# Kernel tuning notes

Hardware: AMD Instinct MI355X
Metric: run time of the kernel (lower is better)

The kernel has to match this reference:

```python
import jax, jax.numpy as jnp
import numpy as np
import math


def setup_inputs() -> dict:
    key = jax.random.key(0)
    ks = jax.random.split(key, 16)
    B, S, H, K, PREV = 32, 2048, 1024, 4, 2
    sc = 0.02
    return {
        "last_hidden": jax.random.normal(ks[0], (1, B, H), jnp.float32),
        "decoder_inputs": jax.random.normal(ks[1], (B, 1, H), jnp.float32),
        "encoder_outputs": jax.random.normal(ks[2], (B, S, H), jnp.float32),
        "attention_scores": jax.random.normal(ks[3], (PREV, B, 1, S), jnp.float32),
        "attention_mask": jnp.zeros((B, 1, S), jnp.float32),
        "evidence_scores": jax.random.uniform(ks[4], (B,), jnp.float32),
        "evidence_sentence_index": jax.random.randint(ks[5], (B, PREV), 0, S, dtype=jnp.int32),
        "W_ih": jax.random.normal(ks[6], (3 * H, H), jnp.float32) * sc,
        "W_hh": jax.random.normal(ks[7], (3 * H, H), jnp.float32) * sc,
        "b_ih": jax.random.normal(ks[8], (3 * H,), jnp.float32) * sc,
        "b_hh": jax.random.normal(ks[9], (3 * H,), jnp.float32) * sc,
        "Wk": jax.random.normal(ks[10], (H, H), jnp.float32) * sc,
        "bk": jnp.zeros((H,), jnp.float32),
        "Wv": jax.random.normal(ks[11], (H, H), jnp.float32) * sc,
        "bv": jnp.zeros((H,), jnp.float32),
        "topk": K,
    }


def _gru_step(x, h, W_ih, W_hh, b_ih, b_hh):
    # x, h: (B, H). PyTorch GRU cell math.
    gi = x @ W_ih.T + b_ih  # (B, 3H)
    gh = h @ W_hh.T + b_hh  # (B, 3H)
    i_r, i_z, i_n = jnp.split(gi, 3, axis=1)
    h_r, h_z, h_n = jnp.split(gh, 3, axis=1)
    r = jax.nn.sigmoid(i_r + h_r)
    z = jax.nn.sigmoid(i_z + h_z)
    n = jnp.tanh(i_n + r * h_n)
    return (1.0 - z) * n + z * h


def reference(last_hidden, decoder_inputs, encoder_outputs, attention_scores,
              attention_mask, evidence_scores, evidence_sentence_index,
              W_ih, W_hh, b_ih, b_hh, Wk, bk, Wv, bv, topk):
    B, S, H = encoder_outputs.shape
    K = topk
    R = B // K  # real batch (beam groups)

    key_eo = encoder_outputs @ Wk.T + bk    # (B, S, H)
    val_eo = encoder_outputs @ Wv.T + bv    # (B, S, H)

    h_new = _gru_step(decoder_inputs[:, 0], last_hidden[0], W_ih, W_hh, b_ih, b_hh)  # (B, H)
    output = h_new[:, None, :]              # (B, 1, H)

    attn_outputs = jnp.einsum('bih,bsh->bis', output, key_eo) / math.sqrt(H) + attention_mask  # (B,1,S)
    attn_alignment = jax.nn.softmax(attn_outputs, axis=-1)
    context = jnp.einsum('bis,bsh->bih', attn_alignment, val_eo)  # (B, 1, H)

    # top-k per beam, then joint rerank over topk*topk candidates per real example
    vals, idx = jax.lax.top_k(attn_alignment.reshape(R, K, S), K)  # (R, K, K), sorted desc
    scores = vals.reshape(B, K)
    sentences = idx.reshape(B, K)
    log_scores = -jnp.log(scores) + evidence_scores[:, None]       # (B, K)

    flat = log_scores.reshape(R, K * K)
    order = jnp.argsort(flat, axis=-1)[:, :K]                      # (R, K) ascending, stable
    new_evidence_scores = jnp.take_along_axis(flat, order, axis=1).reshape(B)
    s_flat = (order // K + jnp.arange(R)[:, None] * K).reshape(B)  # source beam in [0, B)
    r_flat = (order % K).reshape(B)

    sel_sent = sentences[s_flat, r_flat]                           # (B,)
    result = context[s_flat]                                       # (B, 1, H)
    hidden = h_new[s_flat][None]                                   # (1, B, H)
    new_evidence_sentence_index = jnp.concatenate(
        [evidence_sentence_index[s_flat], sel_sent[:, None].astype(evidence_sentence_index.dtype)], axis=1)
    new_attention_scores = jnp.concatenate(
        [attention_scores[:, s_flat], attn_outputs[s_flat][None]], axis=0)  # (prev+1, B, 1, S)
    new_attention_mask = attention_mask[s_flat]                    # (B, 1, S)

    return (result, hidden, new_evidence_sentence_index,
            new_attention_scores, new_attention_mask, new_evidence_scores)
```

## Files before the change

kernel.cpp:

```cpp
#include <hip/hip_runtime.h>
#include <hip/hip_bf16.h>
#include <cfloat>
#include <climits>
#include <cmath>

#define BB 32
#define SS 2048
#define HH 1024
#define KK 4
#define CH 32

__global__ __launch_bounds__(256) void gates_partial(
    const float* __restrict__ x, const float* __restrict__ h_old,
    const float* __restrict__ W_ih, const float* __restrict__ W_hh,
    float* __restrict__ part) {
  int t = threadIdx.x;
  int jb = blockIdx.x;
  int k0 = blockIdx.y * 64;
  bool second = (jb >= 12);
  const float* A = second ? h_old : x;
  const float* W = second ? W_hh : W_ih;
  int j0 = jb * 256;
  int jr = j0 - (second ? 3072 : 0);
  const float* wp = W + (size_t)(jr + t) * HH + k0;
  float acc[32];
#pragma unroll
  for (int b = 0; b < 32; b++) acc[b] = 0.f;
  for (int kk = 0; kk < 64; kk += 4) {
    float4 wv = *(const float4*)(wp + kk);
#pragma unroll
    for (int b = 0; b < 32; b++) {
      float4 a = *(const float4*)(A + (size_t)b * HH + k0 + kk);
      acc[b] += a.x * wv.x + a.y * wv.y + a.z * wv.z + a.w * wv.w;
    }
  }
  float* pb = part + (size_t)blockIdx.y * (32 * 6144) + j0 + t;
#pragma unroll
  for (int b = 0; b < 32; b++) pb[(size_t)b * 6144] = acc[b];
}

__global__ __launch_bounds__(256) void gru_q(
    const float* __restrict__ part, const float* __restrict__ b_ih,
    const float* __restrict__ b_hh, const float* __restrict__ h_old,
    const float* __restrict__ Wk, float* __restrict__ h_new,
    float* __restrict__ qpart2) {
  __shared__ float hs[256];
  int t = threadIdx.x;
  int kc = blockIdx.x, b = blockIdx.y;
  int h = kc * 256 + t;
  float s0 = 0.f, s1 = 0.f, s2 = 0.f, s3 = 0.f, s4 = 0.f, s5 = 0.f;
#pragma unroll
  for (int c = 0; c < 16; c++) {
    const float* p = part + ((size_t)c * 32 + b) * 6144;
    s0 += p[h];
    s1 += p[1024 + h];
    s2 += p[2048 + h];
    s3 += p[3072 + h];
    s4 += p[4096 + h];
    s5 += p[5120 + h];
  }
  float ir = s0 + b_ih[h], iz = s1 + b_ih[1024 + h], in_ = s2 + b_ih[2048 + h];
  float hr = s3 + b_hh[h], hz = s4 + b_hh[1024 + h], hn = s5 + b_hh[2048 + h];
  float r = 1.f / (1.f + expf(-(ir + hr)));
  float z = 1.f / (1.f + expf(-(iz + hz)));
  float n = tanhf(in_ + r * hn);
  float hv = (1.f - z) * n + z * h_old[b * HH + h];
  h_new[b * HH + h] = hv;
  hs[t] = hv;
  __syncthreads();
  float4 acc = make_float4(0.f, 0.f, 0.f, 0.f);
  const float* wbase = Wk + (size_t)kc * 256 * HH + 4 * t;
  for (int k = 0; k < 256; k += 4) {
    float4 w0 = *(const float4*)(wbase + (size_t)(k + 0) * HH);
    float4 w1 = *(const float4*)(wbase + (size_t)(k + 1) * HH);
    float4 w2 = *(const float4*)(wbase + (size_t)(k + 2) * HH);
    float4 w3 = *(const float4*)(wbase + (size_t)(k + 3) * HH);
    float a0 = hs[k], a1 = hs[k + 1], a2 = hs[k + 2], a3 = hs[k + 3];
    acc.x += a0 * w0.x + a1 * w1.x + a2 * w2.x + a3 * w3.x;
    acc.y += a0 * w0.y + a1 * w1.y + a2 * w2.y + a3 * w3.y;
    acc.z += a0 * w0.z + a1 * w1.z + a2 * w2.z + a3 * w3.z;
    acc.w += a0 * w0.w + a1 * w1.w + a2 * w2.w + a3 * w3.w;
  }
  *(float4*)(qpart2 + ((size_t)b * 4 + kc) * HH + 4 * t) = acc;
}

__global__ __launch_bounds__(256, 4) void fused_attn(
    const float* __restrict__ eo, const float* __restrict__ qpart2,
    const float* __restrict__ h_new, const float* __restrict__ bk,
    const float* __restrict__ mask, float* __restrict__ logits,
    float* __restrict__ c0part, float* __restrict__ msum_part) {
  __shared__ float q_lds[HH];
  __shared__ float wred[4];
  __shared__ float cacc[4][1024];
  __shared__ float cms[4][2];
  int b = blockIdx.y, sc = blockIdx.x, t = threadIdx.x;
  int w = t >> 6, lane = t & 63;
  {
    float4 qs = *(const float4*)(qpart2 + ((size_t)b * 4 + 0) * HH + 4 * t);
#pragma unroll
    for (int kc = 1; kc < 4; kc++) {
      float4 v = *(const float4*)(qpart2 + ((size_t)b * 4 + kc) * HH + 4 * t);
      qs.x += v.x; qs.y += v.y; qs.z += v.z; qs.w += v.w;
    }
    *(float4*)&q_lds[4 * t] = qs;
    float4 hv = *(const float4*)(h_new + (size_t)b * HH + 4 * t);
    float4 kv = *(const float4*)(bk + 4 * t);
    float p = hv.x * kv.x + hv.y * kv.y + hv.z * kv.z + hv.w * kv.w;
#pragma unroll
    for (int off = 32; off; off >>= 1) p += __shfl_xor(p, off);
    if (lane == 0) wred[w] = p;
  }
  __syncthreads();
  float hb = wred[0] + wred[1] + wred[2] + wred[3];
  float4 qv[4];
#pragma unroll
  for (int i = 0; i < 4; i++) qv[i] = *(const float4*)&q_lds[(i * 64 + lane) * 4];

  float m = -FLT_MAX, sum = 0.f;
  float4 acc[4];
#pragma unroll
  for (int i = 0; i < 4; i++) acc[i] = make_float4(0.f, 0.f, 0.f, 0.f);
  int rbase = sc * 64 + w * 16;
  for (int tile = 0; tile < 8; tile++) {
    int r0 = rbase + tile * 2;
    float4 rv[2][4];
#pragma unroll
    for (int rr = 0; rr < 2; rr++) {
      const float4* e4 = (const float4*)(eo + ((size_t)b * SS + r0 + rr) * HH);
#pragma unroll
      for (int i = 0; i < 4; i++) rv[rr][i] = e4[i * 64 + lane];
    }
    float p0 = 0.f, p1 = 0.f;
#pragma unroll
    for (int i = 0; i < 4; i++) {
      p0 += rv[0][i].x * qv[i].x + rv[0][i].y * qv[i].y +
            rv[0][i].z * qv[i].z + rv[0][i].w * qv[i].w;
      p1 += rv[1][i].x * qv[i].x + rv[1][i].y * qv[i].y +
            rv[1][i].z * qv[i].z + rv[1][i].w * qv[i].w;
    }
#pragma unroll
    for (int off = 32; off; off >>= 1) {
      p0 += __shfl_xor(p0, off);
      p1 += __shfl_xor(p1, off);
    }
    float lv0 = (p0 + hb) * 0.03125f + mask[(size_t)b * SS + r0];
    float lv1 = (p1 + hb) * 0.03125f + mask[(size_t)b * SS + r0 + 1];
    if (lane == 0) {
      logits[(size_t)b * SS + r0] = lv0;
      logits[(size_t)b * SS + r0 + 1] = lv1;
    }
    float m_new = fmaxf(m, fmaxf(lv0, lv1));
    float scale = expf(m - m_new);
    float w0 = expf(lv0 - m_new), w1 = expf(lv1 - m_new);
    sum = sum * scale + w0 + w1;
#pragma unroll
    for (int i = 0; i < 4; i++) {
      acc[i].x = acc[i].x * scale + w0 * rv[0][i].x + w1 * rv[1][i].x;
      acc[i].y = acc[i].y * scale + w0 * rv[0][i].y + w1 * rv[1][i].y;
      acc[i].z = acc[i].z * scale + w0 * rv[0][i].z + w1 * rv[1][i].z;
      acc[i].w = acc[i].w * scale + w0 * rv[0][i].w + w1 * rv[1][i].w;
    }
    m = m_new;
  }
#pragma unroll
  for (int i = 0; i < 4; i++) *(float4*)&cacc[w][i * 256 + lane * 4] = acc[i];
  if (lane == 0) { cms[w][0] = m; cms[w][1] = sum; }
  __syncthreads();
  float m0 = cms[0][0], m1 = cms[1][0], m2 = cms[2][0], m3 = cms[3][0];
  float mb = fmaxf(fmaxf(m0, m1), fmaxf(m2, m3));
  float wt0 = expf(m0 - mb), wt1 = expf(m1 - mb), wt2 = expf(m2 - mb),
        wt3 = expf(m3 - mb);
  float sb = cms[0][1] * wt0 + cms[1][1] * wt1 + cms[2][1] * wt2 + cms[3][1] * wt3;
  float4 a0 = *(float4*)&cacc[0][4 * t];
  float4 a1 = *(float4*)&cacc[1][4 * t];
  float4 a2 = *(float4*)&cacc[2][4 * t];
  float4 a3 = *(float4*)&cacc[3][4 * t];
  float4 r;
  r.x = wt0 * a0.x + wt1 * a1.x + wt2 * a2.x + wt3 * a3.x;
  r.y = wt0 * a0.y + wt1 * a1.y + wt2 * a2.y + wt3 * a3.y;
  r.z = wt0 * a0.z + wt1 * a1.z + wt2 * a2.z + wt3 * a3.z;
  r.w = wt0 * a0.w + wt1 * a1.w + wt2 * a2.w + wt3 * a3.w;
  *(float4*)(c0part + ((size_t)sc * 32 + b) * 1024 + 4 * t) = r;
  if (t == 0) {
    msum_part[((size_t)sc * 32 + b) * 2 + 0] = mb;
    msum_part[((size_t)sc * 32 + b) * 2 + 1] = sb;
  }
}

__device__ __forceinline__ bool vi_better(float av, int ai, float bv, int bi) {
  return av > bv || (av == bv && ai < bi);
}

__global__ __launch_bounds__(256) void attn_finish(
    const float* __restrict__ c0part, const float* __restrict__ msum_part,
    const float* __restrict__ logits, float* __restrict__ c0,
    float* __restrict__ scores, int* __restrict__ sent) {
  int b = blockIdx.x, t = threadIdx.x;
  float m = -FLT_MAX;
  float ms[CH];
#pragma unroll
  for (int c = 0; c < CH; c++) {
    ms[c] = msum_part[((size_t)c * 32 + b) * 2 + 0];
    m = fmaxf(m, ms[c]);
  }
  float sum = 0.f;
  float wc[CH];
#pragma unroll
  for (int c = 0; c < CH; c++) {
    wc[c] = expf(ms[c] - m);
    sum += msum_part[((size_t)c * 32 + b) * 2 + 1] * wc[c];
  }
  float inv = 1.f / sum;
  float4 a = make_float4(0.f, 0.f, 0.f, 0.f);
#pragma unroll
  for (int c = 0; c < CH; c++) {
    float4 v = *(const float4*)(c0part + ((size_t)c * 32 + b) * 1024 + 4 * t);
    a.x += wc[c] * v.x; a.y += wc[c] * v.y;
    a.z += wc[c] * v.z; a.w += wc[c] * v.w;
  }
  a.x *= inv; a.y *= inv; a.z *= inv; a.w *= inv;
  *(float4*)(c0 + (size_t)b * HH + 4 * t) = a;

  float tv0 = -FLT_MAX, tv1 = -FLT_MAX, tv2 = -FLT_MAX, tv3 = -FLT_MAX;
  int ti0 = INT_MAX, ti1 = INT_MAX, ti2 = INT_MAX, ti3 = INT_MAX;
#pragma unroll
  for (int it = 0; it < 8; it++) {
    int idx = it * 256 + t;
    float v = logits[(size_t)b * SS + idx];
    if (vi_better(v, idx, tv3, ti3)) {
      tv3 = v; ti3 = idx;
      if (vi_better(tv3, ti3, tv2, ti2)) { float fv = tv2; int fi = ti2; tv2 = tv3; ti2 = ti3; tv3 = fv; ti3 = fi; }
      if (vi_better(tv2, ti2, tv1, ti1)) { float fv = tv1; int fi = ti1; tv1 = tv2; ti1 = ti2; tv2 = fv; ti2 = fi; }
      if (vi_better(tv1, ti1, tv0, ti0)) { float fv = tv0; int fi = ti0; tv0 = tv1; ti0 = ti1; tv1 = fv; ti1 = fi; }
    }
  }
  __shared__ float sv[256][4];
  __shared__ int si[256][4];
  sv[t][0] = tv0; sv[t][1] = tv1; sv[t][2] = tv2; sv[t][3] = tv3;
  si[t][0] = ti0; si[t][1] = ti1; si[t][2] = ti2; si[t][3] = ti3;
  __syncthreads();
  for (int off = 128; off; off >>= 1) {
    if (t < off) {
      float bv0 = sv[t + off][0], bv1 = sv[t + off][1], bv2 = sv[t + off][2], bv3 = sv[t + off][3];
      int bi0 = si[t + off][0], bi1 = si[t + off][1], bi2 = si[t + off][2], bi3 = si[t + off][3];
      float mv0, mv1, mv2, mv3; int mi0, mi1, mi2, mi3;
      if (vi_better(tv0, ti0, bv3, bi3)) { mv0 = tv0; mi0 = ti0; } else { mv0 = bv3; mi0 = bi3; }
      if (vi_better(tv1, ti1, bv2, bi2)) { mv1 = tv1; mi1 = ti1; } else { mv1 = bv2; mi1 = bi2; }
      if (vi_better(tv2, ti2, bv1, bi1)) { mv2 = tv2; mi2 = ti2; } else { mv2 = bv1; mi2 = bi1; }
      if (vi_better(tv3, ti3, bv0, bi0)) { mv3 = tv3; mi3 = ti3; } else { mv3 = bv0; mi3 = bi0; }
      if (!vi_better(mv0, mi0, mv2, mi2)) { float fv = mv0; int fi = mi0; mv0 = mv2; mi0 = mi2; mv2 = fv; mi2 = fi; }
      if (!vi_better(mv1, mi1, mv3, mi3)) { float fv = mv1; int fi = mi1; mv1 = mv3; mi1 = mi3; mv3 = fv; mi3 = fi; }
      if (!vi_better(mv0, mi0, mv1, mi1)) { float fv = mv0; int fi = mi0; mv0 = mv1; mi0 = mi1; mv1 = fv; mi1 = fi; }
      if (!vi_better(mv2, mi2, mv3, mi3)) { float fv = mv2; int fi = mi2; mv2 = mv3; mi2 = mi3; mv3 = fv; mi3 = fi; }
      tv0 = mv0; tv1 = mv1; tv2 = mv2; tv3 = mv3;
      ti0 = mi0; ti1 = mi1; ti2 = mi2; ti3 = mi3;
      sv[t][0] = tv0; sv[t][1] = tv1; sv[t][2] = tv2; sv[t][3] = tv3;
      si[t][0] = ti0; si[t][1] = ti1; si[t][2] = ti2; si[t][3] = ti3;
    }
    __syncthreads();
  }
  if (t == 0) {
    scores[b * KK + 0] = expf(tv0 - m) * inv; sent[b * KK + 0] = ti0;
    scores[b * KK + 1] = expf(tv1 - m) * inv; sent[b * KK + 1] = ti1;
    scores[b * KK + 2] = expf(tv2 - m) * inv; sent[b * KK + 2] = ti2;
    scores[b * KK + 3] = expf(tv3 - m) * inv; sent[b * KK + 3] = ti3;
  }
}

__global__ __launch_bounds__(256) void ctx_sel_gather(
    const float* __restrict__ scores, const int* __restrict__ sent,
    const float* __restrict__ evidence, const int* __restrict__ esi,
    const float* __restrict__ Wv, const float* __restrict__ bvec,
    const float* __restrict__ c0, const float* __restrict__ hnew,
    const float* __restrict__ attn_in, const float* __restrict__ logits,
    const float* __restrict__ mask, float* __restrict__ out0,
    float* __restrict__ out1, float* __restrict__ out2,
    float* __restrict__ out3, float* __restrict__ out4,
    float* __restrict__ out5) {
  __shared__ int s_sh;
  int jq = blockIdx.x, b = blockIdx.y, t = threadIdx.x;
  int w = t >> 6, lane = t & 63;
  if (t == 0) {
    int r = b >> 2, j = b & 3;
    float ls[16];
    bool used[16];
    for (int k1 = 0; k1 < 4; k1++)
      for (int k2 = 0; k2 < 4; k2++)
        ls[k1 * 4 + k2] = -logf(scores[(r * 4 + k1) * 4 + k2]) + evidence[r * 4 + k1];
    for (int i = 0; i < 16; i++) used[i] = false;
    int best = 0;
    float bvv = FLT_MAX;
    for (int jj = 0; jj <= j; jj++) {
      best = 0;
      bvv = FLT_MAX;
      for (int i = 0; i < 16; i++)
        if (!used[i] && ls[i] < bvv) { bvv = ls[i]; best = i; }
      used[best] = true;
    }
    int k1 = best >> 2, k2 = best & 3;
    int sSel = r * 4 + k1;
    s_sh = sSel;
    if (jq == 0) {
      out5[b] = bvv;
      out2[b * 3 + 0] = (float)esi[sSel * 2 + 0];
      out2[b * 3 + 1] = (float)esi[sSel * 2 + 1];
      out2[b * 3 + 2] = (float)sent[sSel * 4 + k2];
    }
  }
  __syncthreads();
  int s = s_sh;
  float4 cv[4];
  const float4* c4 = (const float4*)(c0 + (size_t)s * HH);
#pragma unroll
  for (int i = 0; i < 4; i++) cv[i] = c4[i * 64 + lane];
  int jbase = jq * 256 + w * 64;
  for (int rr = 0; rr < 64; rr++) {
    int j = jbase + rr;
    const float4* w4 = (const float4*)(Wv + (size_t)j * HH);
    float p = 0.f;
#pragma unroll
    for (int i = 0; i < 4; i++) {
      float4 wv = w4[i * 64 + lane];
      p += wv.x * cv[i].x + wv.y * cv[i].y + wv.z * cv[i].z + wv.w * cv[i].w;
    }
#pragma unroll
    for (int off = 32; off; off >>= 1) p += __shfl_xor(p, off);
    if (lane == 0) out0[(size_t)b * HH + j] = p + bvec[j];
  }
  out1[(size_t)b * HH + jq * 256 + t] = hnew[(size_t)s * HH + jq * 256 + t];
#pragma unroll
  for (int p = 0; p < 2; p++) {
    *(float2*)(out3 + ((size_t)p * BB + b) * SS + jq * 512 + 2 * t) =
        *(const float2*)(attn_in + ((size_t)p * BB + s) * SS + jq * 512 + 2 * t);
  }
  *(float2*)(out3 + ((size_t)2 * BB + b) * SS + jq * 512 + 2 * t) =
      *(const float2*)(logits + (size_t)s * SS + jq * 512 + 2 * t);
  *(float2*)(out4 + (size_t)b * SS + jq * 512 + 2 * t) =
      *(const float2*)(mask + (size_t)s * SS + jq * 512 + 2 * t);
}

extern "C" void kernel_launch(void* const* d_in, const int* in_sizes, int n_in,
                              void* d_out, int out_size, void* d_ws, size_t ws_size,
                              hipStream_t stream) {
  const float* h_old = (const float*)d_in[0];
  const float* x     = (const float*)d_in[1];
  const float* eo    = (const float*)d_in[2];
  const float* attn_in = (const float*)d_in[3];
  const float* mask  = (const float*)d_in[4];
  const float* evidence = (const float*)d_in[5];
  const int*   esi   = (const int*)d_in[6];
  const float* W_ih  = (const float*)d_in[7];
  const float* W_hh  = (const float*)d_in[8];
  const float* b_ih  = (const float*)d_in[9];
  const float* b_hh  = (const float*)d_in[10];
  const float* Wk    = (const float*)d_in[11];
  const float* bk    = (const float*)d_in[12];
  const float* Wv    = (const float*)d_in[13];
  const float* bv    = (const float*)d_in[14];

  float* w = (float*)d_ws;
  float* h_new  = w + 0;
  float* logits = w + 32768;
  float* scores = w + 98304;
  int*   sent   = (int*)(w + 98432);
  float* c0     = w + 98560;
  float* msum_part = w + 131328;
  float* c0part = w + 133376;
  float* gpart  = w + 1181952;
  float* qpart2 = w + 4327680;

  float* out0 = (float*)d_out;
  float* out1 = out0 + 32768;
  float* out2 = out1 + 32768;
  float* out3 = out2 + 96;
  float* out4 = out3 + 196608;
  float* out5 = out4 + 65536;

  gates_partial<<<dim3(24, 16), 256, 0, stream>>>(x, h_old, W_ih, W_hh, gpart);
  gru_q<<<dim3(4, 32), 256, 0, stream>>>(gpart, b_ih, b_hh, h_old, Wk, h_new, qpart2);
  fused_attn<<<dim3(CH, BB), 256, 0, stream>>>(eo, qpart2, h_new, bk, mask,
                                               logits, c0part, msum_part);
  attn_finish<<<BB, 256, 0, stream>>>(c0part, msum_part, logits, c0, scores, sent);
  ctx_sel_gather<<<dim3(4, BB), 256, 0, stream>>>(
      scores, sent, evidence, esi, Wv, bv, c0, h_new, attn_in, logits, mask,
      out0, out1, out2, out3, out4, out5);
}
```

Measured before the change: 152.5 us.

## Split gru_q and attn_finish across more blocks; relax fused_attn launch bounds

gru_q gains a z grid dimension of 2, so each block computes half of the Wk output columns with float2 loads. The GRU gate math is recomputed in both halves, and only z==0 writes h_new. attn_finish now launches 160 blocks: 128 of them each handle a quarter of the context reduction for one batch row, and 32 do the top-k selection. Both changes aim to fill more compute units in small latency-bound kernels, at the cost of redundant gate and softmax-stat work. The occupancy hint on fused_attn's launch bounds is also removed, which may change its register allocation.

After: 151.1 us. About the same (-0.9%).

```diff
diff --git a/kernel.cpp b/kernel.cpp
--- a/kernel.cpp
+++ b/kernel.cpp
@@ -46,7 +46,7 @@
     float* __restrict__ qpart2) {
   __shared__ float hs[256];
   int t = threadIdx.x;
-  int kc = blockIdx.x, b = blockIdx.y;
+  int kc = blockIdx.x, b = blockIdx.y, z = blockIdx.z;
   int h = kc * 256 + t;
   float s0 = 0.f, s1 = 0.f, s2 = 0.f, s3 = 0.f, s4 = 0.f, s5 = 0.f;
 #pragma unroll
@@ -62,29 +62,27 @@
   float ir = s0 + b_ih[h], iz = s1 + b_ih[1024 + h], in_ = s2 + b_ih[2048 + h];
   float hr = s3 + b_hh[h], hz = s4 + b_hh[1024 + h], hn = s5 + b_hh[2048 + h];
   float r = 1.f / (1.f + expf(-(ir + hr)));
-  float z = 1.f / (1.f + expf(-(iz + hz)));
+  float z_ = 1.f / (1.f + expf(-(iz + hz)));
   float n = tanhf(in_ + r * hn);
-  float hv = (1.f - z) * n + z * h_old[b * HH + h];
-  h_new[b * HH + h] = hv;
+  float hv = (1.f - z_) * n + z_ * h_old[b * HH + h];
+  if (z == 0) h_new[b * HH + h] = hv;
   hs[t] = hv;
   __syncthreads();
-  float4 acc = make_float4(0.f, 0.f, 0.f, 0.f);
-  const float* wbase = Wk + (size_t)kc * 256 * HH + 4 * t;
+  float2 acc = make_float2(0.f, 0.f);
+  const float* wb = Wk + (size_t)kc * 256 * HH + z * 512 + 2 * t;
   for (int k = 0; k < 256; k += 4) {
-    float4 w0 = *(const float4*)(wbase + (size_t)(k + 0) * HH);
-    float4 w1 = *(const float4*)(wbase + (size_t)(k + 1) * HH);
-    float4 w2 = *(const float4*)(wbase + (size_t)(k + 2) * HH);
-    float4 w3 = *(const float4*)(wbase + (size_t)(k + 3) * HH);
+    float2 w0 = *(const float2*)(wb + (size_t)(k + 0) * HH);
+    float2 w1 = *(const float2*)(wb + (size_t)(k + 1) * HH);
+    float2 w2 = *(const float2*)(wb + (size_t)(k + 2) * HH);
+    float2 w3 = *(const float2*)(wb + (size_t)(k + 3) * HH);
     float a0 = hs[k], a1 = hs[k + 1], a2 = hs[k + 2], a3 = hs[k + 3];
     acc.x += a0 * w0.x + a1 * w1.x + a2 * w2.x + a3 * w3.x;
     acc.y += a0 * w0.y + a1 * w1.y + a2 * w2.y + a3 * w3.y;
-    acc.z += a0 * w0.z + a1 * w1.z + a2 * w2.z + a3 * w3.z;
-    acc.w += a0 * w0.w + a1 * w1.w + a2 * w2.w + a3 * w3.w;
-  }
-  *(float4*)(qpart2 + ((size_t)b * 4 + kc) * HH + 4 * t) = acc;
-}
-
-__global__ __launch_bounds__(256, 4) void fused_attn(
+  }
+  *(float2*)(qpart2 + ((size_t)b * 4 + kc) * HH + z * 512 + 2 * t) = acc;
+}
+
+__global__ __launch_bounds__(256) void fused_attn(
     const float* __restrict__ eo, const float* __restrict__ qpart2,
     const float* __restrict__ h_new, const float* __restrict__ bk,
     const float* __restrict__ mask, float* __restrict__ logits,
@@ -195,7 +193,8 @@
     const float* __restrict__ c0part, const float* __restrict__ msum_part,
     const float* __restrict__ logits, float* __restrict__ c0,
     float* __restrict__ scores, int* __restrict__ sent) {
-  int b = blockIdx.x, t = threadIdx.x;
+  int bid = blockIdx.x, t = threadIdx.x;
+  int b = (bid < 128) ? (bid >> 2) : (bid - 128);
   float m = -FLT_MAX;
   float ms[CH];
 #pragma unroll
@@ -211,15 +210,16 @@
     sum += msum_part[((size_t)c * 32 + b) * 2 + 1] * wc[c];
   }
   float inv = 1.f / sum;
-  float4 a = make_float4(0.f, 0.f, 0.f, 0.f);
-#pragma unroll
-  for (int c = 0; c < CH; c++) {
-    float4 v = *(const float4*)(c0part + ((size_t)c * 32 + b) * 1024 + 4 * t);
-    a.x += wc[c] * v.x; a.y += wc[c] * v.y;
-    a.z += wc[c] * v.z; a.w += wc[c] * v.w;
-  }
-  a.x *= inv; a.y *= inv; a.z *= inv; a.w *= inv;
-  *(float4*)(c0 + (size_t)b * HH + 4 * t) = a;
+
+  if (bid < 128) {
+    int h = (bid & 3) * 256 + t;
+    float a = 0.f;
+#pragma unroll
+    for (int c = 0; c < CH; c++)
+      a += wc[c] * c0part[((size_t)c * 32 + b) * 1024 + h];
+    c0[(size_t)b * HH + h] = a * inv;
+    return;
+  }
 
   float tv0 = -FLT_MAX, tv1 = -FLT_MAX, tv2 = -FLT_MAX, tv3 = -FLT_MAX;
   int ti0 = INT_MAX, ti1 = INT_MAX, ti2 = INT_MAX, ti3 = INT_MAX;
@@ -377,10 +377,10 @@
   float* out5 = out4 + 65536;
 
   gates_partial<<<dim3(24, 16), 256, 0, stream>>>(x, h_old, W_ih, W_hh, gpart);
-  gru_q<<<dim3(4, 32), 256, 0, stream>>>(gpart, b_ih, b_hh, h_old, Wk, h_new, qpart2);
+  gru_q<<<dim3(4, 32, 2), 256, 0, stream>>>(gpart, b_ih, b_hh, h_old, Wk, h_new, qpart2);
   fused_attn<<<dim3(CH, BB), 256, 0, stream>>>(eo, qpart2, h_new, bk, mask,
                                                logits, c0part, msum_part);
-  attn_finish<<<BB, 256, 0, stream>>>(c0part, msum_part, logits, c0, scores, sent);
+  attn_finish<<<160, 256, 0, stream>>>(c0part, msum_part, logits, c0, scores, sent);
   ctx_sel_gather<<<dim3(4, BB), 256, 0, stream>>>(
       scores, sent, evidence, esi, Wv, bv, c0, h_new, attn_in, logits, mask,
       out0, out1, out2, out3, out4, out5);
```
